# Kernel optimization log

Measured on AMD Instinct MI355X. Metric: run time of the kernel, lower is better.

Reference implementation:

```python
import jax, jax.numpy as jnp
import numpy as np

B, C, H, W = 16, 256, 64, 64
WS, NH = 8, 4
HD = C // NH
EPS = 1e-5


def setup_inputs() -> dict:
    key = jax.random.key(0)
    ks = jax.random.split(key, 32)
    s = 0.02
    d = {}
    d['x'] = jax.random.normal(ks[0], (B, C, H, W), jnp.float32)
    d['conv1_w'] = jax.random.normal(ks[1], (C, C, 1, 1), jnp.float32) * s
    d['conv1_b'] = jnp.zeros((C,), jnp.float32)
    d['bn1_g'] = jnp.ones((C,), jnp.float32)
    d['bn1_b'] = jnp.zeros((C,), jnp.float32)
    d['bn1_m'] = jax.random.normal(ks[2], (C,), jnp.float32) * 0.1
    d['bn1_v'] = jax.random.uniform(ks[3], (C,), jnp.float32, 0.5, 1.5)
    d['dw_w'] = jax.random.normal(ks[4], (C, 1, 3, 3), jnp.float32) * s
    d['dw_b'] = jnp.zeros((C,), jnp.float32)
    d['bn2_g'] = jnp.ones((C,), jnp.float32)
    d['bn2_b'] = jnp.zeros((C,), jnp.float32)
    d['bn2_m'] = jax.random.normal(ks[5], (C,), jnp.float32) * 0.1
    d['bn2_v'] = jax.random.uniform(ks[6], (C,), jnp.float32, 0.5, 1.5)
    d['conv3_w'] = jax.random.normal(ks[7], (C, C, 1, 1), jnp.float32) * s
    d['conv3_b'] = jnp.zeros((C,), jnp.float32)
    d['ln1_g'] = jnp.ones((C,), jnp.float32)
    d['ln1_b'] = jnp.zeros((C,), jnp.float32)
    d['qkv_w'] = jax.random.normal(ks[8], (3 * C, C), jnp.float32) * s
    d['qkv_b'] = jnp.zeros((3 * C,), jnp.float32)
    d['proj_w'] = jax.random.normal(ks[9], (C, C), jnp.float32) * s
    d['proj_b'] = jnp.zeros((C,), jnp.float32)
    d['ln2_g'] = jnp.ones((C,), jnp.float32)
    d['ln2_b'] = jnp.zeros((C,), jnp.float32)
    d['mlp_w1'] = jax.random.normal(ks[10], (4 * C, C), jnp.float32) * s
    d['mlp_b1'] = jnp.zeros((4 * C,), jnp.float32)
    d['mlp_w2'] = jax.random.normal(ks[11], (C, 4 * C), jnp.float32) * s
    d['mlp_b2'] = jnp.zeros((C,), jnp.float32)
    return d


def _bn(x, g, b, m, v):
    # eval-mode BatchNorm2d over channel dim of NCHW
    inv = g / jnp.sqrt(v + EPS)
    return x * inv[None, :, None, None] + (b - m * inv)[None, :, None, None]


def _ln(x, g, b):
    mu = x.mean(-1, keepdims=True)
    var = ((x - mu) ** 2).mean(-1, keepdims=True)
    return (x - mu) / jnp.sqrt(var + EPS) * g + b


def reference(x, conv1_w, conv1_b, bn1_g, bn1_b, bn1_m, bn1_v, dw_w, dw_b,
              bn2_g, bn2_b, bn2_m, bn2_v, conv3_w, conv3_b, ln1_g, ln1_b,
              qkv_w, qkv_b, proj_w, proj_b, ln2_g, ln2_b,
              mlp_w1, mlp_b1, mlp_w2, mlp_b2):
    # H,W divisible by WS -> no padding
    # conv path: 1x1 -> BN -> dw3x3 -> BN -> 1x1, residual
    h = jnp.einsum('bchw,oc->bohw', x, conv1_w[:, :, 0, 0]) + conv1_b[None, :, None, None]
    h = _bn(h, bn1_g, bn1_b, bn1_m, bn1_v)
    h = jax.lax.conv_general_dilated(h, dw_w, (1, 1), 'SAME',
                                     feature_group_count=C,
                                     dimension_numbers=('NCHW', 'OIHW', 'NCHW'))
    h = h + dw_b[None, :, None, None]
    h = _bn(h, bn2_g, bn2_b, bn2_m, bn2_v)
    h = jnp.einsum('bchw,oc->bohw', h, conv3_w[:, :, 0, 0]) + conv3_b[None, :, None, None]
    x = x + h

    attn_res = x
    # window partition: (B,C,H,W) -> (B*nWin, WS*WS, C)
    w = x.reshape(B, C, H // WS, WS, W // WS, WS)
    w = w.transpose(0, 2, 4, 3, 5, 1).reshape(-1, WS * WS, C)
    w = _ln(w, ln1_g, ln1_b)

    B_, N, _ = w.shape
    qkv = w @ qkv_w.T + qkv_b                      # (B_, N, 3C)
    qkv = qkv.reshape(B_, N, 3, NH, HD).transpose(2, 0, 3, 1, 4)
    q, k, v = qkv[0], qkv[1], qkv[2]               # (B_, NH, N, HD)
    attn = jax.nn.softmax(jnp.einsum('bhnd,bhmd->bhnm', q, k) * (HD ** -0.5), axis=-1)
    o = jnp.einsum('bhnm,bhmd->bhnd', attn, v)
    o = o.transpose(0, 2, 1, 3).reshape(B_, N, C)
    o = o @ proj_w.T + proj_b
    # window reverse
    o = o.reshape(B, H // WS, W // WS, WS, WS, C)
    o = o.transpose(0, 5, 1, 3, 2, 4).reshape(B, C, H, W)
    x = o + attn_res

    ffn_res = x
    t = x.transpose(0, 2, 3, 1)                    # (B,H,W,C)
    t = _ln(t, ln2_g, ln2_b)
    t = jax.nn.gelu(t @ mlp_w1.T + mlp_b1, approximate=False) @ mlp_w2.T + mlp_b2
    x = ffn_res + t.transpose(0, 3, 1, 2)
    return x
```

## Files before the change

kernel.cpp:

```cpp
#include <hip/hip_runtime.h>
#include <hip/hip_bf16.h>

#define EPS 1e-5f

typedef __attribute__((ext_vector_type(8))) short bf16x8;
typedef __attribute__((ext_vector_type(4))) float f32x4;
typedef __attribute__((ext_vector_type(4))) short s16x4;

__device__ __forceinline__ float b2f(ushort u) {
    union { uint i; float f; } v; v.i = ((uint)u) << 16; return v.f;
}
__device__ __forceinline__ ushort f2b(float f) {
    uint x = __float_as_uint(f);
    return (ushort)((x + 0x7fffu + ((x >> 16) & 1u)) >> 16);
}

#define ASYNC16(dst_lds, src_g) \
    __builtin_amdgcn_global_load_lds((const __attribute__((address_space(1))) void*)(src_g), \
                                     (__attribute__((address_space(3))) void*)(dst_lds), 16, 0, 0)

__global__ void k_fold_conv1(const float* __restrict__ w, const float* __restrict__ cb,
                             const float* __restrict__ g, const float* __restrict__ be,
                             const float* __restrict__ mn, const float* __restrict__ vr,
                             ushort* __restrict__ Wf, float* __restrict__ bf) {
    int i = blockIdx.x * 256 + threadIdx.x;
    int o = i >> 8;
    float inv = g[o] * rsqrtf(vr[o] + EPS);
    Wf[i] = f2b(w[i] * inv);
    if ((i & 255) == 0) bf[o] = cb[o] * inv + be[o] - mn[o] * inv;
}

__global__ void k_fold_dw(const float* __restrict__ w, const float* __restrict__ cb,
                          const float* __restrict__ g, const float* __restrict__ be,
                          const float* __restrict__ mn, const float* __restrict__ vr,
                          float* __restrict__ wT, float* __restrict__ bf) {
    int i = blockIdx.x * 256 + threadIdx.x;
    if (i < 2304) {
        int c = i / 9, k = i % 9;
        float inv = g[c] * rsqrtf(vr[c] + EPS);
        wT[k * 256 + c] = w[i] * inv;
    }
    if (i < 256) {
        float inv = g[i] * rsqrtf(vr[i] + EPS);
        bf[i] = cb[i] * inv + be[i] - mn[i] * inv;
    }
}

__global__ void k_cvt_bf16(const float* __restrict__ s, ushort* __restrict__ d, int n) {
    int i = blockIdx.x * 256 + threadIdx.x;
    if (i < n) d[i] = f2b(s[i]);
}

__global__ __launch_bounds__(256)
void k_transpose_in(const float* __restrict__ x, float* __restrict__ R, ushort* __restrict__ A) {
    __shared__ float T[32][33];
    int b = blockIdx.z;
    int hw0 = blockIdx.x * 32, c0 = blockIdx.y * 32;
    int tx = threadIdx.x & 31, ty = threadIdx.x >> 5;
#pragma unroll
    for (int i = 0; i < 4; ++i) {
        int c = ty + i * 8;
        T[c][tx] = x[((size_t)b * 256 + c0 + c) * 4096 + hw0 + tx];
    }
    __syncthreads();
#pragma unroll
    for (int i = 0; i < 4; ++i) {
        int hwl = ty + i * 8;
        float v = T[tx][hwl];
        size_t t = (size_t)b * 4096 + hw0 + hwl;
        R[t * 256 + c0 + tx] = v;
        A[t * 256 + c0 + tx] = f2b(v);
    }
}

template<int EPI>
__global__ __launch_bounds__(256)
void k_gemm_nt(const ushort* __restrict__ A, const ushort* __restrict__ B,
               const float* __restrict__ bias,
               ushort* __restrict__ Co, float* __restrict__ R,
               int M, int N, int K, int ldb) {
    __shared__ ushort As[2][128 * 64];
    __shared__ ushort Bs[2][128 * 64];
    int tid = threadIdx.x;
    int lane = tid & 63, w = tid >> 6;
    int row0 = blockIdx.x * 128, col0 = blockIdx.y * 128;
    int wr = (w >> 1) * 64, wc = (w & 1) * 64;
    f32x4 acc[4][4];
#pragma unroll
    for (int mi = 0; mi < 4; ++mi)
#pragma unroll
        for (int ni = 0; ni < 4; ++ni) acc[mi][ni] = (f32x4){0.f, 0.f, 0.f, 0.f};

    int lr = lane & 15, lk = (lane >> 4) << 3;
    int rin = lane >> 3;
    int cin_sw = (((lane & 7) ^ (rin & 7)) << 3);
    int rxor = (lr & 7) << 3;

#define GSTAGE(buf, k0)                                                                   \
    _Pragma("unroll")                                                                     \
    for (int i = 0; i < 4; ++i) {                                                         \
        int c = (w << 2) + i;                                                             \
        int r = (c << 3) + rin;                                                           \
        ASYNC16(As[buf] + (c << 9), A + (size_t)(row0 + r) * K + (k0) + cin_sw);          \
        ASYNC16(Bs[buf] + (c << 9), B + (size_t)(col0 + r) * ldb + (k0) + cin_sw);        \
    }

    GSTAGE(0, 0);
    __syncthreads();
    int nt = K >> 6;
    for (int t = 0; t < nt; ++t) {
        int cur = t & 1;
        if (t + 1 < nt) { GSTAGE(cur ^ 1, (t + 1) << 6); }
#pragma unroll
        for (int kk = 0; kk < 64; kk += 32) {
            bf16x8 af[4], bfm[4];
#pragma unroll
            for (int mi = 0; mi < 4; ++mi)
                af[mi]  = *(const bf16x8*)(As[cur] + (wr + mi * 16 + lr) * 64 + ((kk + lk) ^ rxor));
#pragma unroll
            for (int ni = 0; ni < 4; ++ni)
                bfm[ni] = *(const bf16x8*)(Bs[cur] + (wc + ni * 16 + lr) * 64 + ((kk + lk) ^ rxor));
#pragma unroll
            for (int mi = 0; mi < 4; ++mi)
#pragma unroll
                for (int ni = 0; ni < 4; ++ni)
                    acc[mi][ni] = __builtin_amdgcn_mfma_f32_16x16x32_bf16(af[mi], bfm[ni], acc[mi][ni], 0, 0, 0);
        }
        __syncthreads();
    }
#undef GSTAGE

    int lg = lane >> 4;
#pragma unroll
    for (int mi = 0; mi < 4; ++mi)
#pragma unroll
        for (int ni = 0; ni < 4; ++ni)
#pragma unroll
            for (int i = 0; i < 4; ++i) {
                int gr = row0 + wr + mi * 16 + lg * 4 + i;
                int gc = col0 + wc + ni * 16 + lr;
                float v = acc[mi][ni][i] + bias[gc];
                if (EPI == 0) {
                    Co[(size_t)gr * N + gc] = f2b(v);
                } else {
                    R[(size_t)gr * 256 + gc] += v;
                }
            }
}

__global__ __launch_bounds__(512)
void k_mlp(const ushort* __restrict__ Aln, const ushort* __restrict__ W1,
           const float* __restrict__ b1, const ushort* __restrict__ W2,
           const float* __restrict__ b2, const float* __restrict__ R,
           float* __restrict__ out) {
    __shared__ ushort As[64 * 256];
    __shared__ ushort Ps[64 * 128];
    const int tid = threadIdx.x, lane = tid & 63, w = tid >> 6;
    const int lr = lane & 15, lg = lane >> 4;
    const int row0 = blockIdx.x << 6;
    const int rxor = (lr & 7) << 3;

    {
        int rin = lane >> 5;
        int slot = lane & 31;
#pragma unroll
        for (int i = 0; i < 4; ++i) {
            int c = (w << 2) + i;
            int r = (c << 1) + rin;
            int src_col = ((slot ^ (r & 7)) << 3);
            ASYNC16(As + (c << 9), Aln + (size_t)(row0 + r) * 256 + src_col);
        }
    }
    __syncthreads();

    f32x4 oacc[4][2];
#pragma unroll
    for (int mf = 0; mf < 4; ++mf)
#pragma unroll
        for (int nf = 0; nf < 2; ++nf) oacc[mf][nf] = (f32x4){0.f, 0.f, 0.f, 0.f};

    for (int hk = 0; hk < 8; ++hk) {
        const int hc0 = hk << 7;
        f32x4 pacc[4];
#pragma unroll
        for (int mf = 0; mf < 4; ++mf) pacc[mf] = (f32x4){0.f, 0.f, 0.f, 0.f};
        const ushort* w1p = W1 + (size_t)(hc0 + w * 16 + lr) * 256 + lg * 8;
#pragma unroll
        for (int ks = 0; ks < 8; ++ks) {
            bf16x8 bW = *(const bf16x8*)(w1p + ks * 32);
#pragma unroll
            for (int mf = 0; mf < 4; ++mf) {
                bf16x8 aA = *(const bf16x8*)(As + (mf * 16 + lr) * 256 + ((ks * 32 + lg * 8) ^ rxor));
                pacc[mf] = __builtin_amdgcn_mfma_f32_16x16x32_bf16(aA, bW, pacc[mf], 0, 0, 0);
            }
        }
        if (hk) __syncthreads();
        float hb = b1[hc0 + w * 16 + lr];
        int hcol = w * 16 + lr;
#pragma unroll
        for (int mf = 0; mf < 4; ++mf)
#pragma unroll
            for (int i = 0; i < 4; ++i) {
                int row = mf * 16 + lg * 4 + i;
                float v = pacc[mf][i] + hb;
                float gl = 0.5f * v * (1.0f + erff(v * 0.70710678118f));
                int col_sw = ((((hcol >> 3) ^ (row & 7)) << 3) | (hcol & 7));
                Ps[row * 128 + col_sw] = f2b(gl);
            }
        __syncthreads();
        const ushort* w2p = W2 + (size_t)(w * 32 + lr) * 1024 + hc0 + lg * 8;
#pragma unroll
        for (int ks = 0; ks < 4; ++ks) {
            bf16x8 pA[4];
#pragma unroll
            for (int mf = 0; mf < 4; ++mf)
                pA[mf] = *(const bf16x8*)(Ps + (mf * 16 + lr) * 128 + ((ks * 32 + lg * 8) ^ rxor));
            bf16x8 w2f0 = *(const bf16x8*)(w2p + ks * 32);
            bf16x8 w2f1 = *(const bf16x8*)(w2p + 16 * 1024 + ks * 32);
#pragma unroll
            for (int mf = 0; mf < 4; ++mf) {
                oacc[mf][0] = __builtin_amdgcn_mfma_f32_16x16x32_bf16(pA[mf], w2f0, oacc[mf][0], 0, 0, 0);
                oacc[mf][1] = __builtin_amdgcn_mfma_f32_16x16x32_bf16(pA[mf], w2f1, oacc[mf][1], 0, 0, 0);
            }
        }
    }
#pragma unroll
    for (int nf = 0; nf < 2; ++nf) {
        int f = w * 32 + nf * 16 + lr;
        float bb = b2[f];
#pragma unroll
        for (int mf = 0; mf < 4; ++mf)
#pragma unroll
            for (int i = 0; i < 4; ++i) {
                int t = row0 + mf * 16 + lg * 4 + i;
                float v = oacc[mf][nf][i] + bb + R[(size_t)t * 256 + f];
                out[((size_t)(t >> 12) * 256 + f) * 4096 + (t & 4095)] = v;
            }
    }
}

__global__ __launch_bounds__(256)
void k_dwconv(const ushort* __restrict__ Hin, const float* __restrict__ wT,
              const float* __restrict__ bf, ushort* __restrict__ Out) {
    int tid = threadIdx.x;
    int pg = blockIdx.x * 8 + (tid >> 5);
    int c0 = (tid & 31) << 3;
    int p0 = pg << 2;
    int b12 = p0 & ~4095;
    int hw = p0 & 4095, h0 = hw >> 6, w0 = hw & 63;

    float wreg[9][8];
#pragma unroll
    for (int k = 0; k < 9; ++k) {
        f32x4 a = *(const f32x4*)(wT + k * 256 + c0);
        f32x4 bq = *(const f32x4*)(wT + k * 256 + c0 + 4);
        wreg[k][0] = a.x; wreg[k][1] = a.y; wreg[k][2] = a.z; wreg[k][3] = a.w;
        wreg[k][4] = bq.x; wreg[k][5] = bq.y; wreg[k][6] = bq.z; wreg[k][7] = bq.w;
    }
    float acc[4][8];
    {
        f32x4 b0 = *(const f32x4*)(bf + c0), b1 = *(const f32x4*)(bf + c0 + 4);
#pragma unroll
        for (int px = 0; px < 4; ++px) {
            acc[px][0] = b0.x; acc[px][1] = b0.y; acc[px][2] = b0.z; acc[px][3] = b0.w;
            acc[px][4] = b1.x; acc[px][5] = b1.y; acc[px][6] = b1.z; acc[px][7] = b1.w;
        }
    }
#pragma unroll
    for (int dy = -1; dy <= 1; ++dy) {
        int hy = h0 + dy;
        if ((unsigned)hy >= 64u) continue;
        const ushort* rp = Hin + (((size_t)(b12 + (hy << 6))) << 8) + c0;
#pragma unroll
        for (int dx = -1; dx <= 4; ++dx) {
            int col = w0 + dx;
            if ((unsigned)col >= 64u) continue;
            bf16x8 v = *(const bf16x8*)(rp + ((size_t)col << 8));
            float vf[8];
#pragma unroll
            for (int j = 0; j < 8; ++j) vf[j] = b2f((ushort)v[j]);
#pragma unroll
            for (int px = 0; px < 4; ++px) {
                int kx = dx - px + 1;
                if (kx < 0 || kx > 2) continue;
                int k = (dy + 1) * 3 + kx;
#pragma unroll
                for (int j = 0; j < 8; ++j) acc[px][j] += vf[j] * wreg[k][j];
            }
        }
    }
#pragma unroll
    for (int px = 0; px < 4; ++px) {
        bf16x8 o;
#pragma unroll
        for (int j = 0; j < 8; ++j) o[j] = (short)f2b(acc[px][j]);
        *(bf16x8*)(Out + (size_t)(p0 + px) * 256 + c0) = o;
    }
}

__global__ __launch_bounds__(256)
void k_ln(const float* __restrict__ R, const float* __restrict__ g,
          const float* __restrict__ be, ushort* __restrict__ O) {
    int lane = threadIdx.x & 63;
    size_t t = (size_t)blockIdx.x * 4 + (threadIdx.x >> 6);
    f32x4 v = *(const f32x4*)(R + t * 256 + lane * 4);
    float s = v.x + v.y + v.z + v.w;
    float q = v.x * v.x + v.y * v.y + v.z * v.z + v.w * v.w;
#pragma unroll
    for (int m = 1; m < 64; m <<= 1) { s += __shfl_xor(s, m, 64); q += __shfl_xor(q, m, 64); }
    float mu = s * (1.f / 256.f);
    float rs = rsqrtf(q * (1.f / 256.f) - mu * mu + EPS);
    int c = lane * 4;
    f32x4 gv = *(const f32x4*)(g + c), bv = *(const f32x4*)(be + c);
    s16x4 o;
    o[0] = (short)f2b((v.x - mu) * rs * gv.x + bv.x);
    o[1] = (short)f2b((v.y - mu) * rs * gv.y + bv.y);
    o[2] = (short)f2b((v.z - mu) * rs * gv.z + bv.z);
    o[3] = (short)f2b((v.w - mu) * rs * gv.w + bv.w);
    *(s16x4*)(O + t * 256 + c) = o;
}

__global__ __launch_bounds__(256)
void k_attn(const ushort* __restrict__ QKV, ushort* __restrict__ O) {
    __shared__ ushort SH[4][64 * 68];
    const int tid = threadIdx.x;
    const int w = tid >> 6, lane = tid & 63;
    const int lr = lane & 15, lg = lane >> 4;
    const int win = blockIdx.x;
    const int b = win >> 6, wh = (win >> 3) & 7, ww = win & 7;
    const int rowbase = (b << 12) + (wh << 9) + (ww << 3);
    const int h = w;

#define TROW(tok) (rowbase + (((tok) >> 3) << 6) + ((tok) & 7))

    bf16x8 qB[4][2], kA[4][2], vR[8];
#pragma unroll
    for (int f = 0; f < 4; ++f) {
        size_t t = (size_t)TROW(f * 16 + lr);
        const ushort* qp = QKV + t * 768 + h * 64 + lg * 8;
#pragma unroll
        for (int ks = 0; ks < 2; ++ks) {
            qB[f][ks] = *(const bf16x8*)(qp + ks * 32);
            kA[f][ks] = *(const bf16x8*)(qp + 256 + ks * 32);
        }
    }
    {
        size_t t = (size_t)TROW(lane);
        const ushort* vp = QKV + t * 768 + 512 + h * 64;
#pragma unroll
        for (int i = 0; i < 8; ++i) vR[i] = *(const bf16x8*)(vp + i * 8);
    }

    f32x4 st[4][4];
#pragma unroll
    for (int kf = 0; kf < 4; ++kf)
#pragma unroll
        for (int qf = 0; qf < 4; ++qf) st[kf][qf] = (f32x4){0.f, 0.f, 0.f, 0.f};
#pragma unroll
    for (int ks = 0; ks < 2; ++ks)
#pragma unroll
        for (int kf = 0; kf < 4; ++kf)
#pragma unroll
            for (int qf = 0; qf < 4; ++qf)
                st[kf][qf] = __builtin_amdgcn_mfma_f32_16x16x32_bf16(kA[kf][ks], qB[qf][ks], st[kf][qf], 0, 0, 0);

    ushort* P = &SH[w][0];
#pragma unroll
    for (int qf = 0; qf < 4; ++qf) {
        float m = -1e30f;
#pragma unroll
        for (int kf = 0; kf < 4; ++kf)
#pragma unroll
            for (int i = 0; i < 4; ++i) m = fmaxf(m, st[kf][qf][i]);
        m = fmaxf(m, __shfl_xor(m, 16, 64));
        m = fmaxf(m, __shfl_xor(m, 32, 64));
        m *= 0.125f;
        float sum = 0.f;
#pragma unroll
        for (int kf = 0; kf < 4; ++kf) {
            f32x4 e;
#pragma unroll
            for (int i = 0; i < 4; ++i) { e[i] = __expf(st[kf][qf][i] * 0.125f - m); sum += e[i]; }
            st[kf][qf] = e;
        }
        sum += __shfl_xor(sum, 16, 64);
        sum += __shfl_xor(sum, 32, 64);
        float rl = 1.f / sum;
#pragma unroll
        for (int kf = 0; kf < 4; ++kf) {
            s16x4 pk;
#pragma unroll
            for (int i = 0; i < 4; ++i) pk[i] = (short)f2b(st[kf][qf][i] * rl);
            *(s16x4*)(P + (qf * 16 + lr) * 68 + kf * 16 + lg * 4) = pk;
        }
    }
    bf16x8 pA[4][2];
#pragma unroll
    for (int mf = 0; mf < 4; ++mf)
#pragma unroll
        for (int ks = 0; ks < 2; ++ks) {
            union { bf16x8 v8; s16x4 v4[2]; } u;
            const ushort* p = P + (mf * 16 + lr) * 68 + ks * 32 + lg * 8;
            u.v4[0] = *(const s16x4*)(p);
            u.v4[1] = *(const s16x4*)(p + 4);
            pA[mf][ks] = u.v8;
        }
    asm volatile("s_waitcnt lgkmcnt(0)" ::: "memory");
    __builtin_amdgcn_sched_barrier(0);
#pragma unroll
    for (int i = 0; i < 8; ++i) {
        union { bf16x8 v8; s16x4 v4[2]; } u; u.v8 = vR[i];
        *(s16x4*)(P + lane * 68 + i * 8) = u.v4[0];
        *(s16x4*)(P + lane * 68 + i * 8 + 4) = u.v4[1];
    }
    asm volatile("s_waitcnt lgkmcnt(0)" ::: "memory");
    __builtin_amdgcn_sched_barrier(0);
    bf16x8 vB[4][2];
#pragma unroll
    for (int nf = 0; nf < 4; ++nf)
#pragma unroll
        for (int ks = 0; ks < 2; ++ks) {
            bf16x8 vb;
#pragma unroll
            for (int j = 0; j < 8; ++j)
                vb[j] = (short)P[(ks * 32 + lg * 8 + j) * 68 + nf * 16 + lr];
            vB[nf][ks] = vb;
        }
    f32x4 o[4][4];
#pragma unroll
    for (int mf = 0; mf < 4; ++mf)
#pragma unroll
        for (int nf = 0; nf < 4; ++nf) o[mf][nf] = (f32x4){0.f, 0.f, 0.f, 0.f};
#pragma unroll
    for (int ks = 0; ks < 2; ++ks)
#pragma unroll
        for (int mf = 0; mf < 4; ++mf)
#pragma unroll
            for (int nf = 0; nf < 4; ++nf)
                o[mf][nf] = __builtin_amdgcn_mfma_f32_16x16x32_bf16(pA[mf][ks], vB[nf][ks], o[mf][nf], 0, 0, 0);
#pragma unroll
    for (int mf = 0; mf < 4; ++mf)
#pragma unroll
        for (int nf = 0; nf < 4; ++nf)
#pragma unroll
            for (int i = 0; i < 4; ++i) {
                int q = mf * 16 + lg * 4 + i;
                int d = nf * 16 + lr;
                O[(size_t)TROW(q) * 256 + h * 64 + d] = f2b(o[mf][nf][i]);
            }
#undef TROW
}

extern "C" void kernel_launch(void* const* d_in, const int* in_sizes, int n_in,
                              void* d_out, int out_size, void* d_ws, size_t ws_size,
                              hipStream_t stream) {
    const float* x       = (const float*)d_in[0];
    const float* conv1_w = (const float*)d_in[1];
    const float* conv1_b = (const float*)d_in[2];
    const float* bn1_g   = (const float*)d_in[3];
    const float* bn1_b   = (const float*)d_in[4];
    const float* bn1_m   = (const float*)d_in[5];
    const float* bn1_v   = (const float*)d_in[6];
    const float* dw_w    = (const float*)d_in[7];
    const float* dw_b    = (const float*)d_in[8];
    const float* bn2_g   = (const float*)d_in[9];
    const float* bn2_b   = (const float*)d_in[10];
    const float* bn2_m   = (const float*)d_in[11];
    const float* bn2_v   = (const float*)d_in[12];
    const float* conv3_w = (const float*)d_in[13];
    const float* conv3_b = (const float*)d_in[14];
    const float* ln1_g   = (const float*)d_in[15];
    const float* ln1_b   = (const float*)d_in[16];
    const float* qkv_w   = (const float*)d_in[17];
    const float* qkv_b   = (const float*)d_in[18];
    const float* proj_w  = (const float*)d_in[19];
    const float* proj_b  = (const float*)d_in[20];
    const float* ln2_g   = (const float*)d_in[21];
    const float* ln2_b   = (const float*)d_in[22];
    const float* mlp_w1  = (const float*)d_in[23];
    const float* mlp_b1  = (const float*)d_in[24];
    const float* mlp_w2  = (const float*)d_in[25];
    const float* mlp_b2  = (const float*)d_in[26];
    float* out = (float*)d_out;

    char* ws = (char*)d_ws;
    float*  R    = (float*)(ws);
    ushort* Abuf = (ushort*)(ws + (64u  << 20));
    ushort* H1   = (ushort*)(ws + (96u  << 20));
    ushort* BIG  = (ushort*)(ws + (128u << 20));
    char* wp = ws + (224u << 20);
    ushort* W1f  = (ushort*)wp; wp += 131072;
    float*  b1f  = (float*)wp;  wp += 1024;
    float*  wdwT = (float*)wp;  wp += 9216;
    float*  bdw  = (float*)wp;  wp += 1024;
    ushort* W3   = (ushort*)wp; wp += 131072;
    ushort* Wqkv = (ushort*)wp; wp += 393216;
    ushort* Wproj= (ushort*)wp; wp += 131072;
    ushort* Wm1  = (ushort*)wp; wp += 524288;
    ushort* Wm2  = (ushort*)wp; wp += 524288;

    k_fold_conv1<<<256, 256, 0, stream>>>(conv1_w, conv1_b, bn1_g, bn1_b, bn1_m, bn1_v, W1f, b1f);
    k_fold_dw<<<9, 256, 0, stream>>>(dw_w, dw_b, bn2_g, bn2_b, bn2_m, bn2_v, wdwT, bdw);
    k_cvt_bf16<<<256, 256, 0, stream>>>(conv3_w, W3, 65536);
    k_cvt_bf16<<<768, 256, 0, stream>>>(qkv_w, Wqkv, 196608);
    k_cvt_bf16<<<256, 256, 0, stream>>>(proj_w, Wproj, 65536);
    k_cvt_bf16<<<1024, 256, 0, stream>>>(mlp_w1, Wm1, 262144);
    k_cvt_bf16<<<1024, 256, 0, stream>>>(mlp_w2, Wm2, 262144);

    k_transpose_in<<<dim3(128, 8, 16), 256, 0, stream>>>(x, R, Abuf);

    k_gemm_nt<0><<<dim3(512, 2), 256, 0, stream>>>(Abuf, W1f, b1f, H1, nullptr, 65536, 256, 256, 256);
    k_dwconv<<<2048, 256, 0, stream>>>(H1, wdwT, bdw, Abuf);
    k_gemm_nt<2><<<dim3(512, 2), 256, 0, stream>>>(Abuf, W3, conv3_b, nullptr, R, 65536, 256, 256, 256);

    k_ln<<<16384, 256, 0, stream>>>(R, ln1_g, ln1_b, Abuf);
    k_gemm_nt<0><<<dim3(512, 6), 256, 0, stream>>>(Abuf, Wqkv, qkv_b, BIG, nullptr, 65536, 768, 256, 256);
    k_attn<<<1024, 256, 0, stream>>>(BIG, H1);
    k_gemm_nt<2><<<dim3(512, 2), 256, 0, stream>>>(H1, Wproj, proj_b, nullptr, R, 65536, 256, 256, 256);

    k_ln<<<16384, 256, 0, stream>>>(R, ln2_g, ln2_b, Abuf);
    k_mlp<<<1024, 512, 0, stream>>>(Abuf, Wm1, mlp_b1, Wm2, mlp_b2, R, out);
}
```

Baseline: 430.9 us.

## Double MLP token tile to 128 and swap operand roles for weight reuse

The fused MLP kernel now handles 128 tokens per block instead of 64, halving the grid. Each wave computes a 64x32 (hidden x token) tile in the first GEMM and a 64x64 (feature x token) tile in the second, with weights as the A operand. This roughly halves global weight traffic per token and raises MFMA work per fragment load. The GELU tile is stored transposed in padded LDS, and the epilogue reads the residual as vectors and writes NCHW output with tokens contiguous across lanes. The cost is more LDS per block (about 100 KB), which likely limits occupancy to one block per CU, plus more accumulator registers.

```diff
diff --git a/kernel.cpp b/kernel.cpp
--- a/kernel.cpp
+++ b/kernel.cpp
@@ -153,19 +153,19 @@
            const float* __restrict__ b1, const ushort* __restrict__ W2,
            const float* __restrict__ b2, const float* __restrict__ R,
            float* __restrict__ out) {
-    __shared__ ushort As[64 * 256];
-    __shared__ ushort Ps[64 * 128];
+    __shared__ ushort As[128 * 256];
+    __shared__ ushort Ps[128 * 136];
     const int tid = threadIdx.x, lane = tid & 63, w = tid >> 6;
     const int lr = lane & 15, lg = lane >> 4;
-    const int row0 = blockIdx.x << 6;
+    const int row0 = blockIdx.x << 7;
     const int rxor = (lr & 7) << 3;
 
     {
         int rin = lane >> 5;
         int slot = lane & 31;
 #pragma unroll
-        for (int i = 0; i < 4; ++i) {
-            int c = (w << 2) + i;
+        for (int i = 0; i < 8; ++i) {
+            int c = (w << 3) + i;
             int r = (c << 1) + rin;
             int src_col = ((slot ^ (r & 7)) << 3);
             ASYNC16(As + (c << 9), Aln + (size_t)(row0 + r) * 256 + src_col);
@@ -173,69 +173,84 @@
     }
     __syncthreads();
 
-    f32x4 oacc[4][2];
+    const int wr1 = (w >> 2) * 64, wc1 = (w & 3) * 32;
+    const int wr2 = (w & 3) * 64, wc2 = (w >> 2) * 64;
+
+    f32x4 oacc[4][4];
 #pragma unroll
     for (int mf = 0; mf < 4; ++mf)
 #pragma unroll
-        for (int nf = 0; nf < 2; ++nf) oacc[mf][nf] = (f32x4){0.f, 0.f, 0.f, 0.f};
+        for (int nf = 0; nf < 4; ++nf) oacc[mf][nf] = (f32x4){0.f, 0.f, 0.f, 0.f};
 
     for (int hk = 0; hk < 8; ++hk) {
         const int hc0 = hk << 7;
-        f32x4 pacc[4];
-#pragma unroll
-        for (int mf = 0; mf < 4; ++mf) pacc[mf] = (f32x4){0.f, 0.f, 0.f, 0.f};
-        const ushort* w1p = W1 + (size_t)(hc0 + w * 16 + lr) * 256 + lg * 8;
-#pragma unroll
-        for (int ks = 0; ks < 8; ++ks) {
-            bf16x8 bW = *(const bf16x8*)(w1p + ks * 32);
-#pragma unroll
-            for (int mf = 0; mf < 4; ++mf) {
-                bf16x8 aA = *(const bf16x8*)(As + (mf * 16 + lr) * 256 + ((ks * 32 + lg * 8) ^ rxor));
-                pacc[mf] = __builtin_amdgcn_mfma_f32_16x16x32_bf16(aA, bW, pacc[mf], 0, 0, 0);
+        f32x4 pacc[4][2];
+#pragma unroll
+        for (int mf = 0; mf < 4; ++mf)
+#pragma unroll
+            for (int nf = 0; nf < 2; ++nf) pacc[mf][nf] = (f32x4){0.f, 0.f, 0.f, 0.f};
+#pragma unroll
+        for (int kk = 0; kk < 8; ++kk) {
+            bf16x8 aW[4], bA[2];
+#pragma unroll
+            for (int mf = 0; mf < 4; ++mf)
+                aW[mf] = *(const bf16x8*)(W1 + (size_t)(hc0 + wr1 + mf * 16 + lr) * 256 + kk * 32 + lg * 8);
+#pragma unroll
+            for (int nf = 0; nf < 2; ++nf)
+                bA[nf] = *(const bf16x8*)(As + (wc1 + nf * 16 + lr) * 256 + ((kk * 32 + lg * 8) ^ rxor));
+#pragma unroll
+            for (int mf = 0; mf < 4; ++mf)
+#pragma unroll
+                for (int nf = 0; nf < 2; ++nf)
+                    pacc[mf][nf] = __builtin_amdgcn_mfma_f32_16x16x32_bf16(aW[mf], bA[nf], pacc[mf][nf], 0, 0, 0);
+        }
+        __syncthreads();
+#pragma unroll
+        for (int mf = 0; mf < 4; ++mf) {
+            f32x4 bv = *(const f32x4*)(b1 + hc0 + wr1 + mf * 16 + lg * 4);
+#pragma unroll
+            for (int nf = 0; nf < 2; ++nf) {
+                s16x4 pk;
+#pragma unroll
+                for (int i = 0; i < 4; ++i) {
+                    float v = pacc[mf][nf][i] + bv[i];
+                    pk[i] = (short)f2b(0.5f * v * (1.0f + erff(v * 0.70710678118f)));
+                }
+                *(s16x4*)(Ps + (wc1 + nf * 16 + lr) * 136 + wr1 + mf * 16 + lg * 4) = pk;
             }
         }
-        if (hk) __syncthreads();
-        float hb = b1[hc0 + w * 16 + lr];
-        int hcol = w * 16 + lr;
-#pragma unroll
-        for (int mf = 0; mf < 4; ++mf)
-#pragma unroll
-            for (int i = 0; i < 4; ++i) {
-                int row = mf * 16 + lg * 4 + i;
-                float v = pacc[mf][i] + hb;
-                float gl = 0.5f * v * (1.0f + erff(v * 0.70710678118f));
-                int col_sw = ((((hcol >> 3) ^ (row & 7)) << 3) | (hcol & 7));
-                Ps[row * 128 + col_sw] = f2b(gl);
-            }
         __syncthreads();
-        const ushort* w2p = W2 + (size_t)(w * 32 + lr) * 1024 + hc0 + lg * 8;
-#pragma unroll
-        for (int ks = 0; ks < 4; ++ks) {
-            bf16x8 pA[4];
+#pragma unroll
+        for (int kk = 0; kk < 4; ++kk) {
+            bf16x8 aW2[4], bP[4];
 #pragma unroll
             for (int mf = 0; mf < 4; ++mf)
-                pA[mf] = *(const bf16x8*)(Ps + (mf * 16 + lr) * 128 + ((ks * 32 + lg * 8) ^ rxor));
-            bf16x8 w2f0 = *(const bf16x8*)(w2p + ks * 32);
-            bf16x8 w2f1 = *(const bf16x8*)(w2p + 16 * 1024 + ks * 32);
-#pragma unroll
-            for (int mf = 0; mf < 4; ++mf) {
-                oacc[mf][0] = __builtin_amdgcn_mfma_f32_16x16x32_bf16(pA[mf], w2f0, oacc[mf][0], 0, 0, 0);
-                oacc[mf][1] = __builtin_amdgcn_mfma_f32_16x16x32_bf16(pA[mf], w2f1, oacc[mf][1], 0, 0, 0);
-            }
-        }
-    }
-#pragma unroll
-    for (int nf = 0; nf < 2; ++nf) {
-        int f = w * 32 + nf * 16 + lr;
-        float bb = b2[f];
-#pragma unroll
-        for (int mf = 0; mf < 4; ++mf)
-#pragma unroll
-            for (int i = 0; i < 4; ++i) {
-                int t = row0 + mf * 16 + lg * 4 + i;
-                float v = oacc[mf][nf][i] + bb + R[(size_t)t * 256 + f];
-                out[((size_t)(t >> 12) * 256 + f) * 4096 + (t & 4095)] = v;
-            }
+                aW2[mf] = *(const bf16x8*)(W2 + (size_t)(wr2 + mf * 16 + lr) * 1024 + hc0 + kk * 32 + lg * 8);
+#pragma unroll
+            for (int nf = 0; nf < 4; ++nf)
+                bP[nf] = *(const bf16x8*)(Ps + (wc2 + nf * 16 + lr) * 136 + kk * 32 + lg * 8);
+#pragma unroll
+            for (int mf = 0; mf < 4; ++mf)
+#pragma unroll
+                for (int nf = 0; nf < 4; ++nf)
+                    oacc[mf][nf] = __builtin_amdgcn_mfma_f32_16x16x32_bf16(aW2[mf], bP[nf], oacc[mf][nf], 0, 0, 0);
+        }
+    }
+    const int bb = row0 >> 12;
+    const int hwbase = row0 & 4095;
+#pragma unroll
+    for (int mf = 0; mf < 4; ++mf) {
+        int f0 = wr2 + mf * 16 + lg * 4;
+        f32x4 b2v = *(const f32x4*)(b2 + f0);
+#pragma unroll
+        for (int nf = 0; nf < 4; ++nf) {
+            int tok = wc2 + nf * 16 + lr;
+            f32x4 rv = *(const f32x4*)(R + (size_t)(row0 + tok) * 256 + f0);
+            int hw = hwbase + tok;
+#pragma unroll
+            for (int i = 0; i < 4; ++i)
+                out[((size_t)(bb * 256 + f0 + i)) * 4096 + hw] = oacc[mf][nf][i] + b2v[i] + rv[i];
+        }
     }
 }
 
@@ -519,5 +534,5 @@
     k_gemm_nt<2><<<dim3(512, 2), 256, 0, stream>>>(H1, Wproj, proj_b, nullptr, R, 65536, 256, 256, 256);
 
     k_ln<<<16384, 256, 0, stream>>>(R, ln2_g, ln2_b, Abuf);
-    k_mlp<<<1024, 512, 0, stream>>>(Abuf, Wm1, mlp_b1, Wm2, mlp_b2, R, out);
-}
+    k_mlp<<<512, 512, 0, stream>>>(Abuf, Wm1, mlp_b1, Wm2, mlp_b2, R, out);
+}
```

After: 503.6 us. 16.9% more time.
